# Optimization experiments

Measured on AMD Instinct MI355X. Metric: run time of the kernel, lower is better.

## Reference

```python
import jax, jax.numpy as jnp
import numpy as np

N = 100000
E = 1600000
IN_DIM = 128
HID = 128
OUT_DIM = 64
ORDER = 4


def setup_inputs() -> dict:
    key = jax.random.key(0)
    ks = jax.random.split(key, 10)
    x = jax.random.normal(ks[0], (N, IN_DIM), dtype=jnp.float32)
    edge_index = jax.random.randint(ks[1], (2, E), 0, N, dtype=jnp.int64)
    gen_edge_index = jax.random.randint(ks[2], (2, E), 0, N, dtype=jnp.int64)
    s = 1.0 / np.sqrt(IN_DIM)
    w_orig = jax.random.normal(ks[3], (ORDER + 1, IN_DIM, HID), dtype=jnp.float32) * s
    b_orig = jax.random.normal(ks[4], (ORDER + 1, HID), dtype=jnp.float32) * s
    w_aug = jax.random.normal(ks[5], (ORDER + 1, IN_DIM, HID), dtype=jnp.float32) * s
    b_aug = jax.random.normal(ks[6], (ORDER + 1, HID), dtype=jnp.float32) * s
    fusion_weight = jnp.ones((2,), dtype=jnp.float32)
    clf_w = jax.random.normal(ks[7], (HID, OUT_DIM), dtype=jnp.float32) / np.sqrt(HID)
    clf_b = jax.random.normal(ks[8], (OUT_DIM,), dtype=jnp.float32) / np.sqrt(HID)
    return {"x": x, "edge_index": edge_index, "gen_edge_index": gen_edge_index,
            "w_orig": w_orig, "b_orig": b_orig, "w_aug": w_aug, "b_aug": b_aug,
            "fusion_weight": fusion_weight, "clf_w": clf_w, "clf_b": clf_b}


def _beta_wavelet(x, edge_index, W, b, num_nodes):
    # add self loops
    loop = jnp.arange(num_nodes, dtype=edge_index.dtype)
    row = jnp.concatenate([edge_index[0], loop])
    col = jnp.concatenate([edge_index[1], loop])
    # symmetric normalization D^{-1/2} A D^{-1/2}
    deg = jax.ops.segment_sum(jnp.ones_like(col, dtype=x.dtype), col, num_segments=num_nodes)
    dinv = jnp.where(deg > 0, deg ** -0.5, 0.0)
    norm = dinv[row] * dinv[col]  # [E+N]
    out = x @ W[0] + b[0]
    Tx = x
    for i in range(1, ORDER + 1):
        msg = norm[:, None] * Tx[row]                      # gather + scale [E+N, D]
        Tx = jax.ops.segment_sum(msg, col, num_segments=num_nodes)  # scatter_add
        out = out + Tx @ W[i] + b[i]
    return jax.nn.relu(out)


def reference(x, edge_index, gen_edge_index, w_orig, b_orig, w_aug, b_aug, fusion_weight, clf_w, clf_b):
    num_nodes = x.shape[0]
    h_orig = _beta_wavelet(x, edge_index, w_orig, b_orig, num_nodes)
    h_aug = _beta_wavelet(x, gen_edge_index, w_aug, b_aug, num_nodes)
    w = jax.nn.softmax(fusion_weight)
    h_final = w[0] * h_orig + w[1] * h_aug
    return h_final @ clf_w + clf_b
```

## Files before the change

### kernel.cpp

```cpp
#include <hip/hip_runtime.h>

#define N_NODES 100000
#define NPAD    100096
#define NE      1600000
#define DIM     128
#define ODIM    64
#define NORDER  4
#define KTOT    640
#define NB      391
#define PB_EDGES 16384
#define PB_BLKS  98

typedef _Float16 h8 __attribute__((ext_vector_type(8)));
typedef float f4 __attribute__((ext_vector_type(4)));

__device__ __forceinline__ float2 up2(unsigned p) {
    union { unsigned u; _Float16 h[2]; } c; c.u = p;
    return make_float2((float)c.h[0], (float)c.h[1]);
}
__device__ __forceinline__ unsigned pk2(float x, float y) {
    union { unsigned u; _Float16 h[2]; } c;
    c.h[0] = (_Float16)x; c.h[1] = (_Float16)y;
    return c.u;
}
__device__ __forceinline__ unsigned short f2hbits(float x) {
    union { _Float16 h; unsigned short s; } c;
    c.h = (_Float16)x;
    return c.s;
}
__device__ __forceinline__ float h2f(unsigned short s) {
    union { unsigned short u; _Float16 h; } c;
    c.u = s;
    return (float)c.h;
}
__device__ __forceinline__ void async_cp16(const void* g, void* l) {
    __builtin_amdgcn_global_load_lds((const __attribute__((address_space(1))) void*)g,
                                     (__attribute__((address_space(3))) void*)l, 16, 0, 0);
}

__global__ __launch_bounds__(256) void hist_edges(const int* __restrict__ e0,
                                                  const int* __restrict__ e1,
                                                  int* __restrict__ bhist) {
    __shared__ int lh[NB];
    int t = threadIdx.x;
    int g = blockIdx.x >= 782;
    int blk = g ? (blockIdx.x - 782) : blockIdx.x;
    const int* colp = (g ? e1 : e0) + NE;
    int* bh = bhist + g * NB;
    for (int i = t; i < NB; i += 256) lh[i] = 0;
    __syncthreads();
    int base = blk * 2048 + t;
#pragma unroll
    for (int j = 0; j < 8; ++j) {
        int e = base + j * 256;
        if (e < NE) atomicAdd(&lh[colp[e] >> 8], 1);
    }
    __syncthreads();
    for (int i = t; i < NB; i += 256) if (lh[i]) atomicAdd(&bh[i], lh[i]);
}

__global__ void wave_scan(const int* __restrict__ in,
                          int* __restrict__ oexcl,
                          int* __restrict__ ocur,
                          int n, int with_cur) {
    int wv = threadIdx.x >> 6, lane = threadIdx.x & 63;
    if (wv >= 2) return;
    const int* I = in + wv * n;
    int* O = oexcl + wv * (n + 1);
    int* C = ocur + wv * n;
    int carry = 0;
    for (int base = 0; base < n; base += 64) {
        int i = base + lane;
        int v = (i < n) ? I[i] : 0;
        int s = v;
#pragma unroll
        for (int off = 1; off < 64; off <<= 1) {
            int x = __shfl_up(s, off, 64);
            if (lane >= off) s += x;
        }
        int excl = carry + s - v;
        if (i < n) {
            O[i] = excl;
            if (with_cur) C[i] = excl;
        }
        carry += __shfl(s, 63, 64);
    }
    if (lane == 0) O[n] = carry;
}

__global__ __launch_bounds__(1024) void part_edges(const int* __restrict__ e0,
                                                   const int* __restrict__ e1,
                                                   int* __restrict__ bcursor,
                                                   unsigned* __restrict__ pairs) {
    __shared__ int lh[NB];
    __shared__ int lpos[NB];
    int t = threadIdx.x;
    int g = blockIdx.x >= PB_BLKS;
    int blk = g ? (blockIdx.x - PB_BLKS) : blockIdx.x;
    const int* rowp = (g ? e1 : e0);
    const int* colp = rowp + NE;
    int* bc = bcursor + g * NB;
    unsigned* pr = pairs + (size_t)g * NE;
    for (int i = t; i < NB; i += 1024) lh[i] = 0;
    __syncthreads();
    int base = blk * PB_EDGES + t;
    int rank[16];
    short bk[16];
    unsigned char lcv[16];
#pragma unroll
    for (int j = 0; j < 16; ++j) {
        int e = base + j * 1024;
        rank[j] = -1;
        if (e < NE) {
            int c = colp[e];
            bk[j] = (short)(c >> 8);
            lcv[j] = (unsigned char)(c & 255);
            rank[j] = atomicAdd(&lh[c >> 8], 1);
        }
    }
    __syncthreads();
    for (int i = t; i < NB; i += 1024) {
        int n = lh[i];
        lpos[i] = n ? atomicAdd(&bc[i], n) : 0;
    }
    __syncthreads();
#pragma unroll
    for (int j = 0; j < 16; ++j) {
        int e = base + j * 1024;
        if (e < NE) {
            int b = bk[j];
            pr[lpos[b] + rank[j]] = ((unsigned)rowp[e] << 8) | lcv[j];
        }
    }
}

__global__ __launch_bounds__(256) void cnt_scan(const unsigned* __restrict__ pairs,
                                                const int* __restrict__ boff,
                                                int* __restrict__ ptrv,
                                                float* __restrict__ dinv,
                                                int* __restrict__ bsum) {
    __shared__ int lcnt[256];
    __shared__ int lscan[256];
    int t = threadIdx.x;
    int g = blockIdx.x >= NB;
    int b = g ? (blockIdx.x - NB) : blockIdx.x;
    const unsigned* pr = pairs + (size_t)g * NE;
    const int* bo = boff + g * (NB + 1);
    int* pv = ptrv + g * (N_NODES + 1);
    float* dv = dinv + g * N_NODES;
    int* bs = bsum + g * NB;
    lcnt[t] = 0;
    __syncthreads();
    int s = bo[b], e = bo[b + 1];
    for (int i = s + t; i < e; i += 256)
        atomicAdd(&lcnt[pr[i] & 255u], 1);
    __syncthreads();
    int v = lcnt[t];
    lscan[t] = v;
    __syncthreads();
    for (int off = 1; off < 256; off <<= 1) {
        int x = (t >= off) ? lscan[t - off] : 0;
        __syncthreads();
        lscan[t] += x;
        __syncthreads();
    }
    int node = (b << 8) + t;
    if (node < N_NODES) {
        pv[node] = lscan[t] - v;
        dv[node] = rsqrtf((float)(v + 1));
    }
    if (t == 255) bs[b] = lscan[255];
}

__global__ __launch_bounds__(256) void scan_addk(int* __restrict__ ptrv,
                                                 const int* __restrict__ bmid) {
    int t = threadIdx.x;
    int g = blockIdx.x >= NB;
    int b = g ? (blockIdx.x - NB) : blockIdx.x;
    int* pv = ptrv + g * (N_NODES + 1);
    const int* bm = bmid + g * (NB + 1);
    int node = (b << 8) + t;
    if (node < N_NODES) pv[node] += bm[b];
    if (b == 0 && t == 0) pv[N_NODES] = NE;
}

__global__ __launch_bounds__(256) void fine_csr(const unsigned* __restrict__ pairs,
                                                const int* __restrict__ boff,
                                                const int* __restrict__ ptrv,
                                                int* __restrict__ srcv) {
    __shared__ int lcnt[256];
    int t = threadIdx.x;
    int g = blockIdx.x >= NB;
    int b = g ? (blockIdx.x - NB) : blockIdx.x;
    const unsigned* pr = pairs + (size_t)g * NE;
    const int* bo = boff + g * (NB + 1);
    const int* pv = ptrv + g * (N_NODES + 1);
    int* sv = srcv + (size_t)g * NE;
    lcnt[t] = 0;
    __syncthreads();
    int s = bo[b], e = bo[b + 1];
    int base = b << 8;
    for (int i = s + t; i < e; i += 256) {
        unsigned pk = pr[i];
        int lc = (int)(pk & 255u);
        int pos = pv[base + lc] + atomicAdd(&lcnt[lc], 1);
        sv[pos] = (int)(pk >> 8);
    }
}

__global__ __launch_bounds__(256) void xcast(const float* __restrict__ x,
                                             unsigned* __restrict__ Tbig) {
    int idx = blockIdx.x * 256 + threadIdx.x;
    if (idx >= NPAD * 64) return;
    int m = idx >> 6, u = idx & 63;
    int e = (m << 7) + u * 2;
    float a = (m < N_NODES) ? x[e]     : 0.f;
    float b = (m < N_NODES) ? x[e + 1] : 0.f;
    Tbig[m * 320 + u] = pk2(a, b);
}

__global__ __launch_bounds__(256) void wcast(const float* __restrict__ Wo,
                                             const float* __restrict__ Wa,
                                             const float* __restrict__ cw,
                                             unsigned short* __restrict__ Wt) {
    int idx = blockIdx.x * 256 + threadIdx.x;
    if (idx >= 2 * 5 * DIM * DIM + ODIM * DIM) return;
    if (idx < 2 * 5 * DIM * DIM) {
        int g   = idx / (5 * DIM * DIM);
        int rem = idx % (5 * DIM * DIM);
        int i   = rem / (DIM * DIM);
        int r2  = rem % (DIM * DIM);
        int k8  = r2 >> 10;
        int n   = (r2 >> 3) & 127;
        int k7  = r2 & 7;
        int k   = k8 * 8 + k7;
        const float* W = g ? Wa : Wo;
        Wt[idx] = f2hbits(W[(i * DIM + k) * DIM + n]);
    } else {
        int j = idx - 2 * 5 * DIM * DIM;
        int n = j >> 7, k = j & 127;
        Wt[idx] = f2hbits(cw[k * ODIM + n]);
    }
}

__global__ __launch_bounds__(256) void propagate(const unsigned* __restrict__ Tin,
                                                 unsigned* __restrict__ Tout,
                                                 const int* __restrict__ ptrv,
                                                 const int* __restrict__ srcv,
                                                 const float* __restrict__ dinv) {
    int gid  = blockIdx.x * 256 + threadIdx.x;
    int lane = threadIdx.x & 63;
    int v    = __builtin_amdgcn_readfirstlane(gid >> 6);
    if (v >= N_NODES) return;
    float dv = dinv[v];
    float2 self = up2(Tin[v * 320 + lane]);
    float ax = dv * dv * self.x;
    float ay = dv * dv * self.y;
    int beg = ptrv[v], end = ptrv[v + 1];
    int k = beg;
    for (; k + 16 <= end; k += 16) {
        int u[16];
#pragma unroll
        for (int j = 0; j < 16; ++j) u[j] = srcv[k + j];
        float2 tt[16];
#pragma unroll
        for (int j = 0; j < 16; ++j) tt[j] = up2(Tin[u[j] * 320 + lane]);
        float w[16];
#pragma unroll
        for (int j = 0; j < 16; ++j) w[j] = dinv[u[j]] * dv;
#pragma unroll
        for (int j = 0; j < 16; ++j) { ax += w[j] * tt[j].x; ay += w[j] * tt[j].y; }
    }
    for (; k + 4 <= end; k += 4) {
        int u[4];
#pragma unroll
        for (int j = 0; j < 4; ++j) u[j] = srcv[k + j];
        float2 tt[4];
#pragma unroll
        for (int j = 0; j < 4; ++j) tt[j] = up2(Tin[u[j] * 320 + lane]);
        float w[4];
#pragma unroll
        for (int j = 0; j < 4; ++j) w[j] = dinv[u[j]] * dv;
#pragma unroll
        for (int j = 0; j < 4; ++j) { ax += w[j] * tt[j].x; ay += w[j] * tt[j].y; }
    }
    for (; k < end; ++k) {
        int u = srcv[k];
        float w = dinv[u] * dv;
        float2 t = up2(Tin[u * 320 + lane]);
        ax += w * t.x; ay += w * t.y;
    }
    Tout[v * 320 + lane] = pk2(ax, ay);
}

__global__ __launch_bounds__(256, 2) void gemmH0(
        const unsigned short* __restrict__ A,
        const unsigned short* __restrict__ Wt,
        const float* __restrict__ bO,
        const float* __restrict__ fw,
        unsigned short* __restrict__ H0) {
    __shared__ unsigned short Bl[DIM * DIM];
    __shared__ float bsl[DIM];
    int t = threadIdx.x;
    int lane = t & 63, wv = t >> 6;
    int m0 = blockIdx.x * 128 + wv * 32;
    int l15 = lane & 15, q = lane >> 4;
    if (t < 128) {
        float s = 0.f;
        for (int i = 0; i <= NORDER; ++i) s += bO[i * DIM + t];
        bsl[t] = s;
    }
    float f0 = fw[0], f1 = fw[1];
    float mx = fmaxf(f0, f1);
    float e0 = expf(f0 - mx), e1 = expf(f1 - mx);
    float sw0 = e0 / (e0 + e1);

    f4 acc[2][8];
#pragma unroll
    for (int mt = 0; mt < 2; ++mt)
#pragma unroll
        for (int nt = 0; nt < 8; ++nt) acc[mt][nt] = (f4)(0.f);

#pragma unroll
    for (int i = 0; i < 5; ++i) {
        const unsigned short* WtI = Wt + (size_t)i * DIM * DIM;
        h8 af[2][4];
#pragma unroll
        for (int mt = 0; mt < 2; ++mt)
#pragma unroll
            for (int kc = 0; kc < 4; ++kc)
                af[mt][kc] = *(const h8*)(A + (size_t)(m0 + mt * 16 + l15) * KTOT
                                            + i * DIM + (kc * 4 + q) * 8);
#pragma unroll
        for (int c = 0; c < 8; ++c) {
            int ci = c * 4 + wv;
            async_cp16(WtI + ci * 512 + lane * 8, &Bl[ci * 512]);
        }
        __syncthreads();
#pragma unroll
        for (int kc = 0; kc < 4; ++kc) {
            int c = kc * 4 + q;
#pragma unroll
            for (int nt = 0; nt < 8; ++nt) {
                h8 bf = *(const h8*)&Bl[(size_t)(c * 128 + nt * 16 + l15) * 8];
                acc[0][nt] = __builtin_amdgcn_mfma_f32_16x16x32_f16(af[0][kc], bf, acc[0][nt], 0, 0, 0);
                acc[1][nt] = __builtin_amdgcn_mfma_f32_16x16x32_f16(af[1][kc], bf, acc[1][nt], 0, 0, 0);
            }
        }
        __syncthreads();
    }
#pragma unroll
    for (int mt = 0; mt < 2; ++mt)
#pragma unroll
        for (int nt = 0; nt < 8; ++nt) {
            float bsv = bsl[nt * 16 + l15];
#pragma unroll
            for (int r = 0; r < 4; ++r) {
                int row = m0 + mt * 16 + q * 4 + r;
                H0[(size_t)row * DIM + nt * 16 + l15] =
                    f2hbits(sw0 * fmaxf(acc[mt][nt][r] + bsv, 0.f));
            }
        }
}

__global__ __launch_bounds__(256, 2) void gemm_fused2(
        const unsigned short* __restrict__ A,
        const unsigned short* __restrict__ Wt,
        const unsigned short* __restrict__ H0,
        const float* __restrict__ bA,
        const float* __restrict__ fw,
        const unsigned short* __restrict__ clfWt,
        const float* __restrict__ clfB,
        float* __restrict__ out) {
    __shared__ unsigned short BlH[DIM * 132];
    __shared__ float bsl[DIM];
    unsigned short* Bl = BlH;
    unsigned short* Hl = BlH;
    int t = threadIdx.x;
    int lane = t & 63, wv = t >> 6;
    int m0 = blockIdx.x * 128 + wv * 32;
    int l15 = lane & 15, q = lane >> 4;
    if (t < 128) {
        float s = 0.f;
        for (int i = 0; i <= NORDER; ++i) s += bA[i * DIM + t];
        bsl[t] = s;
    }
    float f0 = fw[0], f1 = fw[1];
    float mx = fmaxf(f0, f1);
    float e0 = expf(f0 - mx), e1 = expf(f1 - mx);
    float sw1 = e1 / (e0 + e1);

    f4 acc[2][8];
#pragma unroll
    for (int mt = 0; mt < 2; ++mt)
#pragma unroll
        for (int nt = 0; nt < 8; ++nt) acc[mt][nt] = (f4)(0.f);

#pragma unroll
    for (int i = 0; i < 5; ++i) {
        const unsigned short* WtI = Wt + (size_t)i * DIM * DIM;
        h8 af[2][4];
#pragma unroll
        for (int mt = 0; mt < 2; ++mt)
#pragma unroll
            for (int kc = 0; kc < 4; ++kc)
                af[mt][kc] = *(const h8*)(A + (size_t)(m0 + mt * 16 + l15) * KTOT
                                            + i * DIM + (kc * 4 + q) * 8);
#pragma unroll
        for (int c = 0; c < 8; ++c) {
            int ci = c * 4 + wv;
            async_cp16(WtI + ci * 512 + lane * 8, &Bl[ci * 512]);
        }
        __syncthreads();
#pragma unroll
        for (int kc = 0; kc < 4; ++kc) {
            int c = kc * 4 + q;
#pragma unroll
            for (int nt = 0; nt < 8; ++nt) {
                h8 bf = *(const h8*)&Bl[(size_t)(c * 128 + nt * 16 + l15) * 8];
                acc[0][nt] = __builtin_amdgcn_mfma_f32_16x16x32_f16(af[0][kc], bf, acc[0][nt], 0, 0, 0);
                acc[1][nt] = __builtin_amdgcn_mfma_f32_16x16x32_f16(af[1][kc], bf, acc[1][nt], 0, 0, 0);
            }
        }
        __syncthreads();
    }

#pragma unroll
    for (int mt = 0; mt < 2; ++mt)
#pragma unroll
        for (int nt = 0; nt < 8; ++nt) {
            float bsv = bsl[nt * 16 + l15];
            int col = nt * 16 + l15;
#pragma unroll
            for (int r = 0; r < 4; ++r) {
                int lrow = wv * 32 + mt * 16 + q * 4 + r;
                int grow = m0 + mt * 16 + q * 4 + r;
                float h = sw1 * fmaxf(acc[mt][nt][r] + bsv, 0.f)
                        + h2f(H0[(size_t)grow * DIM + col]);
                Hl[lrow * 132 + col] = f2hbits(h);
            }
        }
    __syncthreads();

    f4 o[2][4];
#pragma unroll
    for (int mt = 0; mt < 2; ++mt)
#pragma unroll
        for (int n2 = 0; n2 < 4; ++n2) o[mt][n2] = (f4)(0.f);
#pragma unroll
    for (int kc = 0; kc < 4; ++kc) {
        int c = kc * 4 + q;
        h8 ha[2];
#pragma unroll
        for (int mt = 0; mt < 2; ++mt)
            ha[mt] = *(const h8*)&Hl[(wv * 32 + mt * 16 + l15) * 132 + c * 8];
#pragma unroll
        for (int n2 = 0; n2 < 4; ++n2) {
            h8 bf = *(const h8*)&clfWt[(size_t)(n2 * 16 + l15) * DIM + c * 8];
            o[0][n2] = __builtin_amdgcn_mfma_f32_16x16x32_f16(ha[0], bf, o[0][n2], 0, 0, 0);
            o[1][n2] = __builtin_amdgcn_mfma_f32_16x16x32_f16(ha[1], bf, o[1][n2], 0, 0, 0);
        }
    }
#pragma unroll
    for (int mt = 0; mt < 2; ++mt)
#pragma unroll
        for (int n2 = 0; n2 < 4; ++n2) {
            int col = n2 * 16 + l15;
            float cbv = clfB[col];
#pragma unroll
            for (int r = 0; r < 4; ++r) {
                int row = m0 + mt * 16 + q * 4 + r;
                if (row < N_NODES) out[(size_t)row * ODIM + col] = o[mt][n2][r] + cbv;
            }
        }
}

extern "C" void kernel_launch(void* const* d_in, const int* in_sizes, int n_in,
                              void* d_out, int out_size, void* d_ws, size_t ws_size,
                              hipStream_t stream) {
    const float* x   = (const float*)d_in[0];
    const int*   ei  = (const int*)d_in[1];
    const int*   gi  = (const int*)d_in[2];
    const float* w_o = (const float*)d_in[3];
    const float* b_o = (const float*)d_in[4];
    const float* w_a = (const float*)d_in[5];
    const float* b_a = (const float*)d_in[6];
    const float* fw  = (const float*)d_in[7];
    const float* cw  = (const float*)d_in[8];
    const float* cb  = (const float*)d_in[9];
    float* out = (float*)d_out;

    char* p = (char*)d_ws;
    auto alloc = [&](size_t bytes) {
        void* r = (void*)p;
        p += (bytes + 255) & ~(size_t)255;
        return r;
    };
    unsigned* Tbig = (unsigned*)alloc((size_t)NPAD * 320 * 4);
    unsigned short* H0 = (unsigned short*)alloc((size_t)NPAD * DIM * 2);
    unsigned short* Wt = (unsigned short*)alloc(((size_t)2 * 5 * DIM * DIM + ODIM * DIM) * 2);
    float* dinv  = (float*)alloc((size_t)2 * N_NODES * 4);
    unsigned* pairs = (unsigned*)alloc((size_t)2 * NE * 4);
    int* csr_src = (int*)alloc((size_t)2 * NE * 4);
    int* csr_ptr = (int*)alloc((size_t)2 * (N_NODES + 1) * 4);
    int* bhist   = (int*)alloc((size_t)2 * NB * 4);
    int* boff    = (int*)alloc((size_t)2 * (NB + 1) * 4);
    int* bcursor = (int*)alloc((size_t)2 * NB * 4);
    int* bsum    = (int*)alloc((size_t)2 * NB * 4);
    int* bmid    = (int*)alloc((size_t)2 * (NB + 1) * 4);

    const int gP  = (N_NODES * 64 + 255) / 256;
    const int gX  = (NPAD * 64 + 255) / 256;
    const int gW  = (2 * 5 * DIM * DIM + ODIM * DIM + 255) / 256;
    const int gM  = NPAD / 128;

    xcast<<<gX, 256, 0, stream>>>(x, Tbig);
    wcast<<<gW, 256, 0, stream>>>(w_o, w_a, cw, Wt);

    hipMemsetAsync(bhist, 0, (size_t)2 * NB * 4, stream);
    hist_edges<<<2 * 782, 256, 0, stream>>>(ei, gi, bhist);
    wave_scan<<<1, 128, 0, stream>>>(bhist, boff, bcursor, NB, 1);
    part_edges<<<2 * PB_BLKS, 1024, 0, stream>>>(ei, gi, bcursor, pairs);
    cnt_scan<<<2 * NB, 256, 0, stream>>>(pairs, boff, csr_ptr, dinv, bsum);
    wave_scan<<<1, 128, 0, stream>>>(bsum, bmid, bcursor, NB, 0);
    scan_addk<<<2 * NB, 256, 0, stream>>>(csr_ptr, bmid);
    fine_csr<<<2 * NB, 256, 0, stream>>>(pairs, boff, csr_ptr, csr_src);

    for (int i = 1; i <= NORDER; ++i)
        propagate<<<gP, 256, 0, stream>>>(Tbig + (i - 1) * 64, Tbig + i * 64,
                                          csr_ptr, csr_src, dinv);
    gemmH0<<<gM, 256, 0, stream>>>((const unsigned short*)Tbig, Wt, b_o, fw, H0);

    {
        const int* pv = csr_ptr + (N_NODES + 1);
        const int* sv = csr_src + (size_t)NE;
        const float* dv = dinv + (size_t)N_NODES;
        for (int i = 1; i <= NORDER; ++i)
            propagate<<<gP, 256, 0, stream>>>(Tbig + (i - 1) * 64, Tbig + i * 64,
                                              pv, sv, dv);
    }
    gemm_fused2<<<gM, 256, 0, stream>>>((const unsigned short*)Tbig,
                                        Wt + (size_t)5 * DIM * DIM,
                                        H0, b_a, fw,
                                        Wt + (size_t)2 * 5 * DIM * DIM, cb, out);
}
```

Before: 818.2 us.

## Fuse CSR count, scan and fill into one per-bucket kernel

Merges cnt_scan, the second wave_scan, scan_addk and fine_csr into a single bucket_csr kernel. Each bucket already knows its global start from the bucket offsets, so the per-bucket local scan plus that start gives the final row pointers directly, and the source fill uses shared-memory bases instead of re-reading global pointers. This removes three kernel launches and a second pass over the pairs array. It also raises the gemmH0 occupancy hint from 2 to 3 blocks, which may add register pressure or spills.

```diff
diff --git a/kernel.cpp b/kernel.cpp
--- a/kernel.cpp
+++ b/kernel.cpp
@@ -62,7 +62,7 @@
 __global__ void wave_scan(const int* __restrict__ in,
                           int* __restrict__ oexcl,
                           int* __restrict__ ocur,
-                          int n, int with_cur) {
+                          int n) {
     int wv = threadIdx.x >> 6, lane = threadIdx.x & 63;
     if (wv >= 2) return;
     const int* I = in + wv * n;
@@ -81,7 +81,7 @@
         int excl = carry + s - v;
         if (i < n) {
             O[i] = excl;
-            if (with_cur) C[i] = excl;
+            C[i] = excl;
         }
         carry += __shfl(s, 63, 64);
     }
@@ -134,13 +134,13 @@
     }
 }
 
-__global__ __launch_bounds__(256) void cnt_scan(const unsigned* __restrict__ pairs,
-                                                const int* __restrict__ boff,
-                                                int* __restrict__ ptrv,
-                                                float* __restrict__ dinv,
-                                                int* __restrict__ bsum) {
+__global__ __launch_bounds__(256) void bucket_csr(const unsigned* __restrict__ pairs,
+                                                  const int* __restrict__ boff,
+                                                  int* __restrict__ ptrv,
+                                                  float* __restrict__ dinv,
+                                                  int* __restrict__ srcv) {
     __shared__ int lcnt[256];
-    __shared__ int lscan[256];
+    __shared__ int lbase[256];
     int t = threadIdx.x;
     int g = blockIdx.x >= NB;
     int b = g ? (blockIdx.x - NB) : blockIdx.x;
@@ -148,7 +148,7 @@
     const int* bo = boff + g * (NB + 1);
     int* pv = ptrv + g * (N_NODES + 1);
     float* dv = dinv + g * N_NODES;
-    int* bs = bsum + g * NB;
+    int* sv = srcv + (size_t)g * NE;
     lcnt[t] = 0;
     __syncthreads();
     int s = bo[b], e = bo[b + 1];
@@ -156,54 +156,29 @@
         atomicAdd(&lcnt[pr[i] & 255u], 1);
     __syncthreads();
     int v = lcnt[t];
-    lscan[t] = v;
+    lbase[t] = v;
     __syncthreads();
     for (int off = 1; off < 256; off <<= 1) {
-        int x = (t >= off) ? lscan[t - off] : 0;
+        int x = (t >= off) ? lbase[t - off] : 0;
         __syncthreads();
-        lscan[t] += x;
+        lbase[t] += x;
         __syncthreads();
     }
     int node = (b << 8) + t;
+    int gbase = s + lbase[t] - v;
+    lbase[t] = gbase;
+    lcnt[t] = 0;
     if (node < N_NODES) {
-        pv[node] = lscan[t] - v;
+        pv[node] = gbase;
         dv[node] = rsqrtf((float)(v + 1));
     }
-    if (t == 255) bs[b] = lscan[255];
-}
-
-__global__ __launch_bounds__(256) void scan_addk(int* __restrict__ ptrv,
-                                                 const int* __restrict__ bmid) {
-    int t = threadIdx.x;
-    int g = blockIdx.x >= NB;
-    int b = g ? (blockIdx.x - NB) : blockIdx.x;
-    int* pv = ptrv + g * (N_NODES + 1);
-    const int* bm = bmid + g * (NB + 1);
-    int node = (b << 8) + t;
-    if (node < N_NODES) pv[node] += bm[b];
-    if (b == 0 && t == 0) pv[N_NODES] = NE;
-}
-
-__global__ __launch_bounds__(256) void fine_csr(const unsigned* __restrict__ pairs,
-                                                const int* __restrict__ boff,
-                                                const int* __restrict__ ptrv,
-                                                int* __restrict__ srcv) {
-    __shared__ int lcnt[256];
-    int t = threadIdx.x;
-    int g = blockIdx.x >= NB;
-    int b = g ? (blockIdx.x - NB) : blockIdx.x;
-    const unsigned* pr = pairs + (size_t)g * NE;
-    const int* bo = boff + g * (NB + 1);
-    const int* pv = ptrv + g * (N_NODES + 1);
-    int* sv = srcv + (size_t)g * NE;
-    lcnt[t] = 0;
-    __syncthreads();
-    int s = bo[b], e = bo[b + 1];
-    int base = b << 8;
+    if (b == 0 && g == 0 && t == 0) ptrv[N_NODES] = NE;
+    if (b == 0 && g == 1 && t == 0) ptrv[2 * N_NODES + 1] = NE;
+    __syncthreads();
     for (int i = s + t; i < e; i += 256) {
         unsigned pk = pr[i];
         int lc = (int)(pk & 255u);
-        int pos = pv[base + lc] + atomicAdd(&lcnt[lc], 1);
+        int pos = lbase[lc] + atomicAdd(&lcnt[lc], 1);
         sv[pos] = (int)(pk >> 8);
     }
 }
@@ -293,7 +268,7 @@
     Tout[v * 320 + lane] = pk2(ax, ay);
 }
 
-__global__ __launch_bounds__(256, 2) void gemmH0(
+__global__ __launch_bounds__(256, 3) void gemmH0(
         const unsigned short* __restrict__ A,
         const unsigned short* __restrict__ Wt,
         const float* __restrict__ bO,
@@ -506,8 +481,6 @@
     int* bhist   = (int*)alloc((size_t)2 * NB * 4);
     int* boff    = (int*)alloc((size_t)2 * (NB + 1) * 4);
     int* bcursor = (int*)alloc((size_t)2 * NB * 4);
-    int* bsum    = (int*)alloc((size_t)2 * NB * 4);
-    int* bmid    = (int*)alloc((size_t)2 * (NB + 1) * 4);
 
     const int gP  = (N_NODES * 64 + 255) / 256;
     const int gX  = (NPAD * 64 + 255) / 256;
@@ -519,12 +492,9 @@
 
     hipMemsetAsync(bhist, 0, (size_t)2 * NB * 4, stream);
     hist_edges<<<2 * 782, 256, 0, stream>>>(ei, gi, bhist);
-    wave_scan<<<1, 128, 0, stream>>>(bhist, boff, bcursor, NB, 1);
+    wave_scan<<<1, 128, 0, stream>>>(bhist, boff, bcursor, NB);
     part_edges<<<2 * PB_BLKS, 1024, 0, stream>>>(ei, gi, bcursor, pairs);
-    cnt_scan<<<2 * NB, 256, 0, stream>>>(pairs, boff, csr_ptr, dinv, bsum);
-    wave_scan<<<1, 128, 0, stream>>>(bsum, bmid, bcursor, NB, 0);
-    scan_addk<<<2 * NB, 256, 0, stream>>>(csr_ptr, bmid);
-    fine_csr<<<2 * NB, 256, 0, stream>>>(pairs, boff, csr_ptr, csr_src);
+    bucket_csr<<<2 * NB, 256, 0, stream>>>(pairs, boff, csr_ptr, dinv, csr_src);
 
     for (int i = 1; i <= NORDER; ++i)
         propagate<<<gP, 256, 0, stream>>>(Tbig + (i - 1) * 64, Tbig + i * 64,
```

Result: no change. 809.2 us (-1.1%).
